# Kernel optimization log

Measured on AMD Instinct MI355X. Metric: run time of the kernel, lower is better.

Reference implementation:

```python
import jax, jax.numpy as jnp
import numpy as np

B, S, H, NH = 2, 2048, 1024, 16
HD = H // NH  # 64


def setup_inputs() -> dict:
    key = jax.random.key(0)
    ks = jax.random.split(key, 9)
    w = lambda k: jax.random.normal(k, (H, H), dtype=jnp.float32) * 0.02  # torch Linear weight [out,in]
    b = lambda k: jax.random.normal(k, (H,), dtype=jnp.float32) * 0.02
    return {
        "hidden_states": jax.random.normal(ks[0], (B, S, H), dtype=jnp.float32),
        "Wq": w(ks[1]), "bq": b(ks[2]),
        "Wk": w(ks[3]), "bk": b(ks[4]),
        "Wv": w(ks[5]), "bv": b(ks[6]),
        "Wo": w(ks[7]), "bo": b(ks[8]),
    }


def reference(hidden_states, Wq, bq, Wk, bk, Wv, bv, Wo, bo):
    b, s, h = hidden_states.shape
    nh, hd = NH, h // NH

    def proj(W, bias):
        y = hidden_states @ W.T + bias  # torch Linear: x W^T + b
        return y.reshape(b, s, nh, hd).transpose(0, 2, 1, 3)  # [b, h, s, d]

    q = proj(Wq, bq)
    k = proj(Wk, bk)
    v = proj(Wv, bv)

    scale = jnp.sqrt(jnp.asarray(hd, dtype=q.dtype))
    scores = jnp.einsum("bhqd,bhkd->bhqk", q, k) / scale  # [b, h, s, s]
    pos = jnp.arange(s)
    causal = pos[:, None] < pos[None, :]  # True where masked (key after query)
    scores = jnp.where(causal[None, None], -jnp.inf, scores)
    attn = jax.nn.softmax(scores, axis=-1)
    out = jnp.einsum("bhqk,bhkd->bhqd", attn, v)
    out = out.transpose(0, 2, 1, 3).reshape(b, s, h)
    return out @ Wo.T + bo
```

## Files before the change

kernel.cpp:

```cpp
#include <hip/hip_runtime.h>
#include <stdint.h>

typedef __bf16 bf16;
typedef __attribute__((ext_vector_type(2))) __bf16 bf16x2;
typedef __attribute__((ext_vector_type(4))) __bf16 bf16x4;
typedef __attribute__((ext_vector_type(8))) __bf16 bf16x8;
typedef __attribute__((ext_vector_type(4))) float f32x4;

#define B_  2
#define S_  2048
#define H_  1024
#define NH_ 16
#define HD_ 64
#define ST  72
#define STV 136

__device__ __forceinline__ void glds16(const bf16* g, bf16* l) {
  __builtin_amdgcn_global_load_lds(
      (const __attribute__((address_space(1))) uint32_t*)g,
      (__attribute__((address_space(3))) uint32_t*)l, 16, 0, 0);
}

__global__ __launch_bounds__(256) void cvt_f32_bf16(
    const float* __restrict__ s0, bf16* __restrict__ d0, int n0,
    const float* __restrict__ s1, bf16* __restrict__ d1,
    const float* __restrict__ s2, bf16* __restrict__ d2,
    const float* __restrict__ s3, bf16* __restrict__ d3,
    const float* __restrict__ s4, bf16* __restrict__ d4, int nw)
{
  const float* s; bf16* d; int n;
  switch (blockIdx.y) {
    case 0:  s = s0; d = d0; n = n0; break;
    case 1:  s = s1; d = d1; n = nw; break;
    case 2:  s = s2; d = d2; n = nw; break;
    case 3:  s = s3; d = d3; n = nw; break;
    default: s = s4; d = d4; n = nw; break;
  }
  const int i = (blockIdx.x * 256 + threadIdx.x) * 8;
  if (i >= n) return;
  float4 v0 = *(const float4*)(s + i);
  float4 v1 = *(const float4*)(s + i + 4);
  bf16x8 o;
  o[0] = (bf16)v0.x; o[1] = (bf16)v0.y; o[2] = (bf16)v0.z; o[3] = (bf16)v0.w;
  o[4] = (bf16)v1.x; o[5] = (bf16)v1.y; o[6] = (bf16)v1.z; o[7] = (bf16)v1.w;
  *(bf16x8*)(d + i) = o;
}

template <typename TY>
__global__ __launch_bounds__(256) void gemm_bt_bias(
    const bf16* __restrict__ X,
    const bf16* __restrict__ W0, const bf16* __restrict__ W1, const bf16* __restrict__ W2,
    const float* __restrict__ b0, const float* __restrict__ b1, const float* __restrict__ b2,
    TY* __restrict__ Y0, TY* __restrict__ Y1, TY* __restrict__ Y2,
    int M, int N, int K)
{
  const bf16* W; const float* bias; TY* Y;
  if (blockIdx.z == 0)      { W = W0; bias = b0; Y = Y0; }
  else if (blockIdx.z == 1) { W = W1; bias = b1; Y = Y1; }
  else                      { W = W2; bias = b2; Y = Y2; }

  __shared__ __align__(16) bf16 As[2][64 * 32];
  __shared__ __align__(16) bf16 Bs[2][128 * 32];

  const int tid  = threadIdx.x;
  const int lane = tid & 63;
  const int wave = tid >> 6;
  const int quad = lane >> 4;
  const int l15  = lane & 15;
  const int m0 = blockIdx.y * 64;
  const int n0 = blockIdx.x * 128;
  const int wm = (wave >> 1) * 32;
  const int wn = (wave & 1) * 64;

  const int ar = tid >> 2,           ac = (tid & 3) * 8;
  const int br0 = tid >> 2,          bc0 = (tid & 3) * 8;
  const int br1 = (256 + tid) >> 2,  bc1 = ((256 + tid) & 3) * 8;
  const int abase  = wave * 512;
  const int bbase0 = wave * 512;
  const int bbase1 = 2048 + wave * 512;

  f32x4 acc[2][4] = {};

  glds16(X + (size_t)(m0 + ar) * K + ac,  &As[0][abase]);
  glds16(W + (size_t)(n0 + br0) * K + bc0, &Bs[0][bbase0]);
  glds16(W + (size_t)(n0 + br1) * K + bc1, &Bs[0][bbase1]);

  int pb = 0;
  for (int k0 = 0; k0 < K; k0 += 32, pb ^= 1) {
    __syncthreads();

    if (k0 + 32 < K) {
      const int kn = k0 + 32;
      glds16(X + (size_t)(m0 + ar) * K + kn + ac,  &As[pb ^ 1][abase]);
      glds16(W + (size_t)(n0 + br0) * K + kn + bc0, &Bs[pb ^ 1][bbase0]);
      glds16(W + (size_t)(n0 + br1) * K + kn + bc1, &Bs[pb ^ 1][bbase1]);
    }

    bf16x8 a[2], b[4];
#pragma unroll
    for (int i = 0; i < 2; ++i)
      a[i] = *(const bf16x8*)&As[pb][(wm + i * 16 + l15) * 32 + quad * 8];
#pragma unroll
    for (int i = 0; i < 4; ++i)
      b[i] = *(const bf16x8*)&Bs[pb][(wn + i * 16 + l15) * 32 + quad * 8];
#pragma unroll
    for (int mi = 0; mi < 2; ++mi)
#pragma unroll
      for (int ni = 0; ni < 4; ++ni)
        acc[mi][ni] = __builtin_amdgcn_mfma_f32_16x16x32_bf16(a[mi], b[ni], acc[mi][ni], 0, 0, 0);
  }

#pragma unroll
  for (int mi = 0; mi < 2; ++mi) {
    const int row = m0 + wm + mi * 16 + quad * 4;
#pragma unroll
    for (int ni = 0; ni < 4; ++ni) {
      const int col = n0 + wn + ni * 16 + l15;
      const float bv = bias[col];
#pragma unroll
      for (int r = 0; r < 4; ++r)
        Y[(size_t)(row + r) * N + col] = (TY)(acc[mi][ni][r] + bv);
    }
  }
}

__global__ __launch_bounds__(256) void attn_causal(
    const bf16* __restrict__ Q, const bf16* __restrict__ K,
    const bf16* __restrict__ V, bf16* __restrict__ O)
{
  const int bh   = blockIdx.x;
  const int pair = blockIdx.y;
  const int b    = bh >> 4;
  const int h    = bh & 15;

  const int tid  = threadIdx.x;
  const int lane = tid & 63;
  const int wave = tid >> 6;
  const int quad = lane >> 4;
  const int l15  = lane & 15;
  const size_t headoff = (size_t)b * S_ * H_ + (size_t)h * HD_;
  const float SCL = 0.125f * 1.44269504f;

  __shared__ __align__(16) bf16 Qs[64 * ST];
  __shared__ __align__(16) bf16 Ks[128 * ST];
  __shared__ __align__(16) bf16 Vt[64 * STV];
  __shared__ __align__(16) bf16 Ps[4][16 * STV];

  for (int phase = 0; phase < 2; ++phase) {
    const int qt = phase ? (31 - pair) : pair;
    const int q0 = qt * 64;
    __syncthreads();

#pragma unroll
    for (int it = 0; it < 2; ++it) {
      const int c = it * 256 + tid, row = c >> 3, col = (c & 7) * 8;
      *(bf16x8*)&Qs[row * ST + col] =
          *(const bf16x8*)(Q + headoff + (size_t)(q0 + row) * H_ + col);
    }

    const int qrow = q0 + wave * 16 + l15;
    float mr = -1e30f, lr = 0.0f;
    f32x4 oacc[4] = {};

    const int niter = (qt >> 1) + 1;
    for (int it = 0; it < niter; ++it) {
      const int k0 = it * 128;
      __syncthreads();

#pragma unroll
      for (int j = 0; j < 4; ++j) {
        const int c = j * 256 + tid, row = c >> 3, col = (c & 7) * 8;
        *(bf16x8*)&Ks[row * ST + col] =
            *(const bf16x8*)(K + headoff + (size_t)(k0 + row) * H_ + col);
      }
      {
        const int vr = (tid & 63) * 2;
        const int vc = (tid >> 6) * 16;
        bf16x8 a0 = *(const bf16x8*)(V + headoff + (size_t)(k0 + vr) * H_ + vc);
        bf16x8 a1 = *(const bf16x8*)(V + headoff + (size_t)(k0 + vr) * H_ + vc + 8);
        bf16x8 c0 = *(const bf16x8*)(V + headoff + (size_t)(k0 + vr + 1) * H_ + vc);
        bf16x8 c1 = *(const bf16x8*)(V + headoff + (size_t)(k0 + vr + 1) * H_ + vc + 8);
#pragma unroll
        for (int e = 0; e < 8; ++e) {
          bf16x2 p0; p0[0] = a0[e]; p0[1] = c0[e];
          *(bf16x2*)&Vt[(vc + e) * STV + vr] = p0;
          bf16x2 p1; p1[0] = a1[e]; p1[1] = c1[e];
          *(bf16x2*)&Vt[(vc + 8 + e) * STV + vr] = p1;
        }
      }
      __syncthreads();

      f32x4 sacc[8] = {};
#pragma unroll
      for (int ks = 0; ks < 2; ++ks) {
        bf16x8 bq = *(const bf16x8*)&Qs[(wave * 16 + l15) * ST + ks * 32 + quad * 8];
#pragma unroll
        for (int mb = 0; mb < 8; ++mb) {
          bf16x8 ak = *(const bf16x8*)&Ks[(mb * 16 + l15) * ST + ks * 32 + quad * 8];
          sacc[mb] = __builtin_amdgcn_mfma_f32_16x16x32_bf16(ak, bq, sacc[mb], 0, 0, 0);
        }
      }

      float sv[8][4];
      if (it == niter - 1) {
#pragma unroll
        for (int mb = 0; mb < 8; ++mb) {
          const int kb = k0 + mb * 16 + quad * 4;
#pragma unroll
          for (int r = 0; r < 4; ++r) {
            const float s = sacc[mb][r] * SCL;
            sv[mb][r] = (kb + r > qrow) ? -1e30f : s;
          }
        }
      } else {
#pragma unroll
        for (int mb = 0; mb < 8; ++mb)
#pragma unroll
          for (int r = 0; r < 4; ++r)
            sv[mb][r] = sacc[mb][r] * SCL;
      }

      float mx = -1e30f;
#pragma unroll
      for (int mb = 0; mb < 8; ++mb)
        mx = fmaxf(mx, fmaxf(fmaxf(sv[mb][0], sv[mb][1]), fmaxf(sv[mb][2], sv[mb][3])));
      mx = fmaxf(mx, __shfl_xor(mx, 16, 64));
      mx = fmaxf(mx, __shfl_xor(mx, 32, 64));
      const float mnew  = fmaxf(mr, mx);
      const float alpha = __builtin_amdgcn_exp2f(mr - mnew);
      mr = mnew;

      float sum = 0.0f;
#pragma unroll
      for (int mb = 0; mb < 8; ++mb) {
        bf16x4 pw;
#pragma unroll
        for (int r = 0; r < 4; ++r) {
          const float p = __builtin_amdgcn_exp2f(sv[mb][r] - mnew);
          sum += p;
          pw[r] = (bf16)p;
        }
        *(bf16x4*)&Ps[wave][l15 * STV + mb * 16 + quad * 4] = pw;
      }
      sum += __shfl_xor(sum, 16, 64);
      sum += __shfl_xor(sum, 32, 64);
      lr = lr * alpha + sum;
#pragma unroll
      for (int mb = 0; mb < 4; ++mb)
#pragma unroll
        for (int r = 0; r < 4; ++r) oacc[mb][r] *= alpha;

#pragma unroll
      for (int ks = 0; ks < 4; ++ks) {
        bf16x8 bp = *(const bf16x8*)&Ps[wave][l15 * STV + ks * 32 + quad * 8];
#pragma unroll
        for (int mb = 0; mb < 4; ++mb) {
          bf16x8 av = *(const bf16x8*)&Vt[(mb * 16 + l15) * STV + ks * 32 + quad * 8];
          oacc[mb] = __builtin_amdgcn_mfma_f32_16x16x32_bf16(av, bp, oacc[mb], 0, 0, 0);
        }
      }
    }

    const float inv = 1.0f / lr;
#pragma unroll
    for (int mb = 0; mb < 4; ++mb) {
      bf16x4 o;
#pragma unroll
      for (int r = 0; r < 4; ++r) o[r] = (bf16)(oacc[mb][r] * inv);
      *(bf16x4*)(O + headoff + (size_t)qrow * H_ + mb * 16 + quad * 4) = o;
    }
  }
}

extern "C" void kernel_launch(void* const* d_in, const int* in_sizes, int n_in,
                              void* d_out, int out_size, void* d_ws, size_t ws_size,
                              hipStream_t stream) {
  const float* hs = (const float*)d_in[0];
  const float* Wq = (const float*)d_in[1]; const float* bq = (const float*)d_in[2];
  const float* Wk = (const float*)d_in[3]; const float* bk = (const float*)d_in[4];
  const float* Wv = (const float*)d_in[5]; const float* bv = (const float*)d_in[6];
  const float* Wo = (const float*)d_in[7]; const float* bo = (const float*)d_in[8];
  float* out = (float*)d_out;

  const size_t elems = (size_t)B_ * S_ * H_;
  const size_t wel   = (size_t)H_ * H_;
  bf16* hsb = (bf16*)d_ws;
  bf16* AO  = hsb;
  bf16* Wqb = hsb + elems;
  bf16* Wkb = Wqb + wel;
  bf16* Wvb = Wkb + wel;
  bf16* Wob = Wvb + wel;
  bf16* Qw  = Wob + wel;
  bf16* Kw  = Qw + elems;
  bf16* Vw  = Kw + elems;

  cvt_f32_bf16<<<dim3(2048, 5), dim3(256), 0, stream>>>(
      hs, hsb, (int)elems, Wq, Wqb, Wk, Wkb, Wv, Wvb, Wo, Wob, (int)wel);

  const int M = B_ * S_;
  gemm_bt_bias<bf16><<<dim3(H_ / 128, M / 64, 3), dim3(256), 0, stream>>>(
      hsb, Wqb, Wkb, Wvb, bq, bk, bv, Qw, Kw, Vw, M, H_, H_);

  attn_causal<<<dim3(B_ * NH_, 16), dim3(256), 0, stream>>>(Qw, Kw, Vw, AO);

  gemm_bt_bias<float><<<dim3(H_ / 128, M / 64, 1), dim3(256), 0, stream>>>(
      AO, Wob, Wob, Wob, bo, bo, bo, out, out, out, M, H_, H_);
}
```

Before: 212.3 us.

## Halve wave count, double per-wave tiles, and emit V pre-transposed from QKV GEMM

The QKV GEMM now writes V directly in a per-head transposed [b,h,d,s] layout, so the attention kernel loads V^T with plain vector copies instead of doing a register shuffle into LDS. Both the GEMMs and the attention kernel drop to 128 threads per block, with each wave covering twice as many rows (4x4 MFMA tiles in the GEMM, two 16-row query groups in attention). This raises MFMA work per LDS fragment load and removes the transpose scatter, but halves the waves per block and increases register pressure, which may reduce occupancy and latency hiding.

```diff
diff --git a/kernel.cpp b/kernel.cpp
--- a/kernel.cpp
+++ b/kernel.cpp
@@ -2,7 +2,6 @@
 #include <stdint.h>
 
 typedef __bf16 bf16;
-typedef __attribute__((ext_vector_type(2))) __bf16 bf16x2;
 typedef __attribute__((ext_vector_type(4))) __bf16 bf16x4;
 typedef __attribute__((ext_vector_type(8))) __bf16 bf16x8;
 typedef __attribute__((ext_vector_type(4))) float f32x4;
@@ -46,8 +45,8 @@
   *(bf16x8*)(d + i) = o;
 }
 
-template <typename TY>
-__global__ __launch_bounds__(256) void gemm_bt_bias(
+template <typename TY, bool VT2>
+__global__ __launch_bounds__(128) void gemm_bt_bias(
     const bf16* __restrict__ X,
     const bf16* __restrict__ W0, const bf16* __restrict__ W1, const bf16* __restrict__ W2,
     const float* __restrict__ b0, const float* __restrict__ b1, const float* __restrict__ b2,
@@ -69,64 +68,85 @@
   const int l15  = lane & 15;
   const int m0 = blockIdx.y * 64;
   const int n0 = blockIdx.x * 128;
-  const int wm = (wave >> 1) * 32;
-  const int wn = (wave & 1) * 64;
-
-  const int ar = tid >> 2,           ac = (tid & 3) * 8;
-  const int br0 = tid >> 2,          bc0 = (tid & 3) * 8;
-  const int br1 = (256 + tid) >> 2,  bc1 = ((256 + tid) & 3) * 8;
-  const int abase  = wave * 512;
-  const int bbase0 = wave * 512;
-  const int bbase1 = 2048 + wave * 512;
-
-  f32x4 acc[2][4] = {};
-
-  glds16(X + (size_t)(m0 + ar) * K + ac,  &As[0][abase]);
-  glds16(W + (size_t)(n0 + br0) * K + bc0, &Bs[0][bbase0]);
-  glds16(W + (size_t)(n0 + br1) * K + bc1, &Bs[0][bbase1]);
+  const int wn = wave * 64;
+
+  f32x4 acc[4][4] = {};
+
+#define GLDS_A(buf, koff)                                                     \
+  _Pragma("unroll") for (int it = 0; it < 2; ++it) {                          \
+    const int c = it * 128 + tid;                                             \
+    glds16(X + (size_t)(m0 + (c >> 2)) * K + (koff) + (c & 3) * 8,            \
+           &As[buf][(it * 128 + wave * 64) * 8]);                             \
+  }
+#define GLDS_B(buf, koff)                                                     \
+  _Pragma("unroll") for (int it = 0; it < 4; ++it) {                          \
+    const int c = it * 128 + tid;                                             \
+    glds16(W + (size_t)(n0 + (c >> 2)) * K + (koff) + (c & 3) * 8,            \
+           &Bs[buf][(it * 128 + wave * 64) * 8]);                             \
+  }
+
+  GLDS_A(0, 0)
+  GLDS_B(0, 0)
 
   int pb = 0;
   for (int k0 = 0; k0 < K; k0 += 32, pb ^= 1) {
     __syncthreads();
 
     if (k0 + 32 < K) {
-      const int kn = k0 + 32;
-      glds16(X + (size_t)(m0 + ar) * K + kn + ac,  &As[pb ^ 1][abase]);
-      glds16(W + (size_t)(n0 + br0) * K + kn + bc0, &Bs[pb ^ 1][bbase0]);
-      glds16(W + (size_t)(n0 + br1) * K + kn + bc1, &Bs[pb ^ 1][bbase1]);
-    }
-
-    bf16x8 a[2], b[4];
-#pragma unroll
-    for (int i = 0; i < 2; ++i)
-      a[i] = *(const bf16x8*)&As[pb][(wm + i * 16 + l15) * 32 + quad * 8];
+      GLDS_A(pb ^ 1, k0 + 32)
+      GLDS_B(pb ^ 1, k0 + 32)
+    }
+
+    bf16x8 a[4], b[4];
+#pragma unroll
+    for (int i = 0; i < 4; ++i)
+      a[i] = *(const bf16x8*)&As[pb][(i * 16 + l15) * 32 + quad * 8];
 #pragma unroll
     for (int i = 0; i < 4; ++i)
       b[i] = *(const bf16x8*)&Bs[pb][(wn + i * 16 + l15) * 32 + quad * 8];
 #pragma unroll
-    for (int mi = 0; mi < 2; ++mi)
+    for (int mi = 0; mi < 4; ++mi)
 #pragma unroll
       for (int ni = 0; ni < 4; ++ni)
         acc[mi][ni] = __builtin_amdgcn_mfma_f32_16x16x32_bf16(a[mi], b[ni], acc[mi][ni], 0, 0, 0);
   }
-
-#pragma unroll
-  for (int mi = 0; mi < 2; ++mi) {
-    const int row = m0 + wm + mi * 16 + quad * 4;
-#pragma unroll
-    for (int ni = 0; ni < 4; ++ni) {
-      const int col = n0 + wn + ni * 16 + l15;
-      const float bv = bias[col];
-#pragma unroll
-      for (int r = 0; r < 4; ++r)
-        Y[(size_t)(row + r) * N + col] = (TY)(acc[mi][ni][r] + bv);
-    }
-  }
-}
-
-__global__ __launch_bounds__(256) void attn_causal(
+#undef GLDS_A
+#undef GLDS_B
+
+  if (VT2 && blockIdx.z == 2) {
+#pragma unroll
+    for (int mi = 0; mi < 4; ++mi) {
+      const int row0 = m0 + mi * 16 + quad * 4;
+      const int bb = row0 >> 11, s0 = row0 & 2047;
+#pragma unroll
+      for (int ni = 0; ni < 4; ++ni) {
+        const int col = n0 + wn + ni * 16 + l15;
+        const float bv = bias[col];
+        bf16x4 o;
+#pragma unroll
+        for (int r = 0; r < 4; ++r) o[r] = (bf16)(acc[mi][ni][r] + bv);
+        *(bf16x4*)((bf16*)Y + ((size_t)(bb << 4 << 6) + col) * S_ + s0) = o;
+      }
+    }
+  } else {
+#pragma unroll
+    for (int mi = 0; mi < 4; ++mi) {
+      const int row = m0 + mi * 16 + quad * 4;
+#pragma unroll
+      for (int ni = 0; ni < 4; ++ni) {
+        const int col = n0 + wn + ni * 16 + l15;
+        const float bv = bias[col];
+#pragma unroll
+        for (int r = 0; r < 4; ++r)
+          Y[(size_t)(row + r) * N + col] = (TY)(acc[mi][ni][r] + bv);
+      }
+    }
+  }
+}
+
+__global__ __launch_bounds__(128) void attn_causal(
     const bf16* __restrict__ Q, const bf16* __restrict__ K,
-    const bf16* __restrict__ V, bf16* __restrict__ O)
+    const bf16* __restrict__ Vt_g, bf16* __restrict__ O)
 {
   const int bh   = blockIdx.x;
   const int pair = blockIdx.y;
@@ -139,12 +159,13 @@
   const int quad = lane >> 4;
   const int l15  = lane & 15;
   const size_t headoff = (size_t)b * S_ * H_ + (size_t)h * HD_;
+  const size_t vhead   = (size_t)bh * 64 * S_;
   const float SCL = 0.125f * 1.44269504f;
 
   __shared__ __align__(16) bf16 Qs[64 * ST];
   __shared__ __align__(16) bf16 Ks[128 * ST];
   __shared__ __align__(16) bf16 Vt[64 * STV];
-  __shared__ __align__(16) bf16 Ps[4][16 * STV];
+  __shared__ __align__(16) bf16 Ps[2][32 * STV];
 
   for (int phase = 0; phase < 2; ++phase) {
     const int qt = phase ? (31 - pair) : pair;
@@ -152,15 +173,14 @@
     __syncthreads();
 
 #pragma unroll
-    for (int it = 0; it < 2; ++it) {
-      const int c = it * 256 + tid, row = c >> 3, col = (c & 7) * 8;
+    for (int it = 0; it < 4; ++it) {
+      const int c = it * 128 + tid, row = c >> 3, col = (c & 7) * 8;
       *(bf16x8*)&Qs[row * ST + col] =
           *(const bf16x8*)(Q + headoff + (size_t)(q0 + row) * H_ + col);
     }
 
-    const int qrow = q0 + wave * 16 + l15;
-    float mr = -1e30f, lr = 0.0f;
-    f32x4 oacc[4] = {};
+    float mr[2] = {-1e30f, -1e30f}, lr[2] = {0.0f, 0.0f};
+    f32x4 oacc[4][2] = {};
 
     const int niter = (qt >> 1) + 1;
     for (int it = 0; it < niter; ++it) {
@@ -168,106 +188,114 @@
       __syncthreads();
 
 #pragma unroll
-      for (int j = 0; j < 4; ++j) {
-        const int c = j * 256 + tid, row = c >> 3, col = (c & 7) * 8;
+      for (int j = 0; j < 8; ++j) {
+        const int c = j * 128 + tid, row = c >> 3, col = (c & 7) * 8;
         *(bf16x8*)&Ks[row * ST + col] =
             *(const bf16x8*)(K + headoff + (size_t)(k0 + row) * H_ + col);
       }
-      {
-        const int vr = (tid & 63) * 2;
-        const int vc = (tid >> 6) * 16;
-        bf16x8 a0 = *(const bf16x8*)(V + headoff + (size_t)(k0 + vr) * H_ + vc);
-        bf16x8 a1 = *(const bf16x8*)(V + headoff + (size_t)(k0 + vr) * H_ + vc + 8);
-        bf16x8 c0 = *(const bf16x8*)(V + headoff + (size_t)(k0 + vr + 1) * H_ + vc);
-        bf16x8 c1 = *(const bf16x8*)(V + headoff + (size_t)(k0 + vr + 1) * H_ + vc + 8);
-#pragma unroll
-        for (int e = 0; e < 8; ++e) {
-          bf16x2 p0; p0[0] = a0[e]; p0[1] = c0[e];
-          *(bf16x2*)&Vt[(vc + e) * STV + vr] = p0;
-          bf16x2 p1; p1[0] = a1[e]; p1[1] = c1[e];
-          *(bf16x2*)&Vt[(vc + 8 + e) * STV + vr] = p1;
-        }
+#pragma unroll
+      for (int j = 0; j < 8; ++j) {
+        const int c = j * 128 + tid, row = c >> 4, col = (c & 15) * 8;
+        *(bf16x8*)&Vt[row * STV + col] =
+            *(const bf16x8*)(Vt_g + vhead + (size_t)row * S_ + k0 + col);
       }
       __syncthreads();
 
-      f32x4 sacc[8] = {};
+      f32x4 sacc[8][2] = {};
 #pragma unroll
       for (int ks = 0; ks < 2; ++ks) {
-        bf16x8 bq = *(const bf16x8*)&Qs[(wave * 16 + l15) * ST + ks * 32 + quad * 8];
+        bf16x8 bq[2];
+#pragma unroll
+        for (int nb = 0; nb < 2; ++nb)
+          bq[nb] = *(const bf16x8*)&Qs[(wave * 32 + nb * 16 + l15) * ST + ks * 32 + quad * 8];
 #pragma unroll
         for (int mb = 0; mb < 8; ++mb) {
           bf16x8 ak = *(const bf16x8*)&Ks[(mb * 16 + l15) * ST + ks * 32 + quad * 8];
-          sacc[mb] = __builtin_amdgcn_mfma_f32_16x16x32_bf16(ak, bq, sacc[mb], 0, 0, 0);
+          sacc[mb][0] = __builtin_amdgcn_mfma_f32_16x16x32_bf16(ak, bq[0], sacc[mb][0], 0, 0, 0);
+          sacc[mb][1] = __builtin_amdgcn_mfma_f32_16x16x32_bf16(ak, bq[1], sacc[mb][1], 0, 0, 0);
         }
       }
 
-      float sv[8][4];
-      if (it == niter - 1) {
+      const bool lastit = (it == niter - 1);
+#pragma unroll
+      for (int nb = 0; nb < 2; ++nb) {
+        const int qrow = q0 + wave * 32 + nb * 16 + l15;
+        float sv[8][4];
+        if (lastit) {
+#pragma unroll
+          for (int mb = 0; mb < 8; ++mb) {
+            const int kb = k0 + mb * 16 + quad * 4;
+#pragma unroll
+            for (int r = 0; r < 4; ++r) {
+              const float s = sacc[mb][nb][r] * SCL;
+              sv[mb][r] = (kb + r > qrow) ? -1e30f : s;
+            }
+          }
+        } else {
+#pragma unroll
+          for (int mb = 0; mb < 8; ++mb)
+#pragma unroll
+            for (int r = 0; r < 4; ++r)
+              sv[mb][r] = sacc[mb][nb][r] * SCL;
+        }
+
+        float mx = -1e30f;
+#pragma unroll
+        for (int mb = 0; mb < 8; ++mb)
+          mx = fmaxf(mx, fmaxf(fmaxf(sv[mb][0], sv[mb][1]), fmaxf(sv[mb][2], sv[mb][3])));
+        mx = fmaxf(mx, __shfl_xor(mx, 16, 64));
+        mx = fmaxf(mx, __shfl_xor(mx, 32, 64));
+        const float mnew  = fmaxf(mr[nb], mx);
+        const float alpha = __builtin_amdgcn_exp2f(mr[nb] - mnew);
+        mr[nb] = mnew;
+
+        float sum = 0.0f;
 #pragma unroll
         for (int mb = 0; mb < 8; ++mb) {
-          const int kb = k0 + mb * 16 + quad * 4;
+          bf16x4 pw;
 #pragma unroll
           for (int r = 0; r < 4; ++r) {
-            const float s = sacc[mb][r] * SCL;
-            sv[mb][r] = (kb + r > qrow) ? -1e30f : s;
+            const float p = __builtin_amdgcn_exp2f(sv[mb][r] - mnew);
+            sum += p;
+            pw[r] = (bf16)p;
           }
+          *(bf16x4*)&Ps[wave][(nb * 16 + l15) * STV + mb * 16 + quad * 4] = pw;
         }
-      } else {
-#pragma unroll
-        for (int mb = 0; mb < 8; ++mb)
-#pragma unroll
-          for (int r = 0; r < 4; ++r)
-            sv[mb][r] = sacc[mb][r] * SCL;
-      }
-
-      float mx = -1e30f;
-#pragma unroll
-      for (int mb = 0; mb < 8; ++mb)
-        mx = fmaxf(mx, fmaxf(fmaxf(sv[mb][0], sv[mb][1]), fmaxf(sv[mb][2], sv[mb][3])));
-      mx = fmaxf(mx, __shfl_xor(mx, 16, 64));
-      mx = fmaxf(mx, __shfl_xor(mx, 32, 64));
-      const float mnew  = fmaxf(mr, mx);
-      const float alpha = __builtin_amdgcn_exp2f(mr - mnew);
-      mr = mnew;
-
-      float sum = 0.0f;
-#pragma unroll
-      for (int mb = 0; mb < 8; ++mb) {
-        bf16x4 pw;
-#pragma unroll
-        for (int r = 0; r < 4; ++r) {
-          const float p = __builtin_amdgcn_exp2f(sv[mb][r] - mnew);
-          sum += p;
-          pw[r] = (bf16)p;
-        }
-        *(bf16x4*)&Ps[wave][l15 * STV + mb * 16 + quad * 4] = pw;
-      }
-      sum += __shfl_xor(sum, 16, 64);
-      sum += __shfl_xor(sum, 32, 64);
-      lr = lr * alpha + sum;
-#pragma unroll
-      for (int mb = 0; mb < 4; ++mb)
-#pragma unroll
-        for (int r = 0; r < 4; ++r) oacc[mb][r] *= alpha;
+        sum += __shfl_xor(sum, 16, 64);
+        sum += __shfl_xor(sum, 32, 64);
+        lr[nb] = lr[nb] * alpha + sum;
+#pragma unroll
+        for (int mb = 0; mb < 4; ++mb)
+#pragma unroll
+          for (int r = 0; r < 4; ++r) oacc[mb][nb][r] *= alpha;
+      }
 
 #pragma unroll
       for (int ks = 0; ks < 4; ++ks) {
-        bf16x8 bp = *(const bf16x8*)&Ps[wave][l15 * STV + ks * 32 + quad * 8];
+        bf16x8 bp[2];
+#pragma unroll
+        for (int nb = 0; nb < 2; ++nb)
+          bp[nb] = *(const bf16x8*)&Ps[wave][(nb * 16 + l15) * STV + ks * 32 + quad * 8];
 #pragma unroll
         for (int mb = 0; mb < 4; ++mb) {
           bf16x8 av = *(const bf16x8*)&Vt[(mb * 16 + l15) * STV + ks * 32 + quad * 8];
-          oacc[mb] = __builtin_amdgcn_mfma_f32_16x16x32_bf16(av, bp, oacc[mb], 0, 0, 0);
+          oacc[mb][0] = __builtin_amdgcn_mfma_f32_16x16x32_bf16(av, bp[0], oacc[mb][0], 0, 0, 0);
+          oacc[mb][1] = __builtin_amdgcn_mfma_f32_16x16x32_bf16(av, bp[1], oacc[mb][1], 0, 0, 0);
         }
       }
     }
 
-    const float inv = 1.0f / lr;
-#pragma unroll
-    for (int mb = 0; mb < 4; ++mb) {
-      bf16x4 o;
-#pragma unroll
-      for (int r = 0; r < 4; ++r) o[r] = (bf16)(oacc[mb][r] * inv);
-      *(bf16x4*)(O + headoff + (size_t)qrow * H_ + mb * 16 + quad * 4) = o;
+#pragma unroll
+    for (int nb = 0; nb < 2; ++nb) {
+      const int qrow = q0 + wave * 32 + nb * 16 + l15;
+      const float inv = 1.0f / lr[nb];
+#pragma unroll
+      for (int mb = 0; mb < 4; ++mb) {
+        bf16x4 o;
+#pragma unroll
+        for (int r = 0; r < 4; ++r) o[r] = (bf16)(oacc[mb][nb][r] * inv);
+        *(bf16x4*)(O + headoff + (size_t)qrow * H_ + mb * 16 + quad * 4) = o;
+      }
     }
   }
 }
@@ -298,11 +326,11 @@
       hs, hsb, (int)elems, Wq, Wqb, Wk, Wkb, Wv, Wvb, Wo, Wob, (int)wel);
 
   const int M = B_ * S_;
-  gemm_bt_bias<bf16><<<dim3(H_ / 128, M / 64, 3), dim3(256), 0, stream>>>(
+  gemm_bt_bias<bf16, true><<<dim3(H_ / 128, M / 64, 3), dim3(128), 0, stream>>>(
       hsb, Wqb, Wkb, Wvb, bq, bk, bv, Qw, Kw, Vw, M, H_, H_);
 
-  attn_causal<<<dim3(B_ * NH_, 16), dim3(256), 0, stream>>>(Qw, Kw, Vw, AO);
-
-  gemm_bt_bias<float><<<dim3(H_ / 128, M / 64, 1), dim3(256), 0, stream>>>(
+  attn_causal<<<dim3(B_ * NH_, 16), dim3(128), 0, stream>>>(Qw, Kw, Vw, AO);
+
+  gemm_bt_bias<float, false><<<dim3(H_ / 128, M / 64, 1), dim3(128), 0, stream>>>(
       AO, Wob, Wob, Wob, bo, bo, bo, out, out, out, M, H_, H_);
 }
```

Result: no change. 208.2 us (-1.9%).
